# Performance work log

Measured on AMD Instinct MI355X. Metric: run time of the kernel, lower is better.

## Reference

```python
import jax, jax.numpy as jnp
import numpy as np

# ---- constants from init_kwargs ----
RES = 128                       # config.grid.resolution (base_resolution, n_levels=1)
LOG2_T = 22
TABLE_SIZE = 1 << LOG2_T        # hashmap entries
N_G = 4                         # features per level, gaussian grid
N_V = 8                         # features per level, vmf grid
BB_MIN = jnp.array([-10.0, -10.0, -10.0], dtype=jnp.float32)
BB_MAX = jnp.array([10.0, 10.0, 10.0], dtype=jnp.float32)
N_PTS = 1048576

_P2 = np.uint32(2654435761)
_P3 = np.uint32(805459861)
# 8 trilinear corner offsets [8,3]
_CORNERS = jnp.array([[i, j, k] for i in (0, 1) for j in (0, 1) for k in (0, 1)], dtype=jnp.int32)


def hashgrid_lookup(table, pos):
    """tcnn-style HashGrid (1 level, trilinear). pos: [N,3] in [0,1] domain."""
    x = pos * RES                     # scale to grid coords
    x0 = jnp.floor(x)
    w = x - x0                        # [N,3] trilinear weights
    corners = x0.astype(jnp.int32)[:, None, :] + _CORNERS[None]   # [N,8,3]
    cu = corners.astype(jnp.uint32)
    h = (cu[..., 0] ^ (cu[..., 1] * _P2) ^ (cu[..., 2] * _P3)) & jnp.uint32(TABLE_SIZE - 1)
    feat = table[h.astype(jnp.int32)]                              # [N,8,F] gather
    wts = jnp.prod(jnp.where(_CORNERS[None].astype(bool), w[:, None, :], 1.0 - w[:, None, :]), axis=-1)  # [N,8]
    return jnp.einsum('nc,ncf->nf', wts, feat)                     # [N,F]


def sample_vpls(pos, gauss_table, vmf_table):
    """Accumulate encodings over the 27-neighbor stencil (accumulate_gaussians=True)."""
    block = 1.0 / RES
    npos = (pos - BB_MIN) / (BB_MAX - BB_MIN)      # normalized [N,3]
    total_g = jnp.zeros((pos.shape[0], N_G), dtype=jnp.float32)
    total_v = jnp.zeros((pos.shape[0], N_V), dtype=jnp.float32)
    for dx in (-1, 0, 1):
        for dy in (-1, 0, 1):
            for dz in (-1, 0, 1):
                off = jnp.array([dx, dy, dz], dtype=jnp.float32) * block
                p = npos + off
                total_g = total_g + hashgrid_lookup(gauss_table, p)
                total_v = total_v + hashgrid_lookup(vmf_table, p)
    return total_g, total_v


def encode(gaussians, vmf):
    # gaussian_mean_encoding='sigmoid' (non-raw -> rescale to bbox)
    mean = jax.nn.sigmoid(gaussians[:, :3]) * (BB_MAX - BB_MIN) + BB_MIN
    variance = jax.nn.softplus(gaussians[:, 3])[:, None]          # 'softplus'
    sharpness = jnp.exp(vmf[:, 0])[:, None]                        # 'exp'
    ax = vmf[:, 1:4]                                               # 'normalize' (F.normalize, eps=1e-12)
    axis = ax / jnp.maximum(jnp.linalg.norm(ax, axis=1, keepdims=True), 1e-12)
    amplitude = jax.nn.sigmoid(vmf[:, 4:7])                        # 'sigmoid'
    g_out = jnp.concatenate([mean, variance], axis=1)             # [N,4]
    v_out = jnp.concatenate([sharpness, axis, amplitude], axis=1) # [N,7]
    return g_out, v_out


def setup_inputs() -> dict:
    key = jax.random.key(0)
    k1, k2, k3 = jax.random.split(key, 3)
    # world-space query positions inside the bounding box
    u = jax.random.uniform(k1, (N_PTS, 3), dtype=jnp.float32)
    pos = u * (BB_MAX - BB_MIN) + BB_MIN
    # hash-grid feature tables (tcnn initializes near zero)
    gauss_table = jax.random.normal(k2, (TABLE_SIZE, N_G), dtype=jnp.float32) * 0.1
    vmf_table = jax.random.normal(k3, (TABLE_SIZE, N_V), dtype=jnp.float32) * 0.1
    return {"pos": pos, "gauss_table": gauss_table, "vmf_table": vmf_table}


def reference(pos, gauss_table, vmf_table):
    gaussians, vmf = sample_vpls(pos, gauss_table, vmf_table)
    return encode(gaussians, vmf)
```

## Files before the change

### kernel.cpp

```cpp
#include <hip/hip_runtime.h>
#include <hip/hip_fp16.h>
#include <cstdint>

#define TABLE_MASK 0x3FFFFFu
#define P2 2654435761u
#define P3 805459861u

#define XD 128
#define YD 132
#define ZD 132
#define RECU 12
#define NB3 (128 * 128 * 8)
#define SCAN_BLKS (NB3 / 1024)
#define BUILD_BLKS (131 * 66)

__device__ __forceinline__ float sigmoidf_(float x) { return 1.0f / (1.0f + expf(-x)); }

__device__ __forceinline__ uint32_t f2h2(float a, float b) {
    __half2 h = __floats2half2_rn(a, b);
    return *reinterpret_cast<uint32_t*>(&h);
}
__device__ __forceinline__ __half2 u2h2(uint32_t u) {
    return *reinterpret_cast<__half2*>(&u);
}

__device__ __forceinline__ int bin_key3(float px, float py, float pz)
{
    float x = ((px + 10.0f) / 20.0f) * 128.0f;
    float y = ((py + 10.0f) / 20.0f) * 128.0f;
    float z = ((pz + 10.0f) / 20.0f) * 128.0f;
    int ix = min(max((int)floorf(x), 0), 127);
    int iy = min(max((int)floorf(y), 0), 127);
    int iz = min(max((int)floorf(z), 0), 127);
    return (((iz << 7) + iy) << 3) + (ix >> 4);
}

__global__ __launch_bounds__(256)
void build_hist_kernel(const float4* __restrict__ gauss,
                       const float4* __restrict__ vmf,
                       uint32_t* __restrict__ exdx,
                       const float* __restrict__ pos,
                       uint32_t* __restrict__ hist, int n)
{
    if (blockIdx.x >= BUILD_BLKS) {
        int p = (blockIdx.x - BUILD_BLKS) * blockDim.x + threadIdx.x;
        if (p < n) {
            int k = bin_key3(pos[3 * p], pos[3 * p + 1], pos[3 * p + 2]);
            atomicAdd(&hist[k], 1u);
        }
        return;
    }

    __shared__ float sm[2][131][13];
    int bidx = blockIdx.x;
    int yp = bidx % 66;
    int rz = 1 + bidx / 66;
    int ry0 = 1 + 2 * yp;
    int t = threadIdx.x;

    for (int l = t; l < 262; l += 256) {
        int row = (l >= 131) ? 1 : 0;
        int cell = l - row * 131;
        int ry = ry0 + row;
        if (ry <= 131) {
            int xc = 1 + cell;
            uint32_t ux = (uint32_t)(xc - 2);
            uint32_t uy = (uint32_t)(ry - 2);
            uint32_t uz = (uint32_t)(rz - 2);
            uint32_t h = (ux ^ (uy * P2) ^ (uz * P3)) & TABLE_MASK;
            float4 g  = gauss[h];
            float4 v0 = vmf[(size_t)2 * h];
            float4 v1 = vmf[(size_t)2 * h + 1];
            float* s = sm[row][cell];
            s[0] = g.x;  s[1] = g.y;  s[2]  = g.z;  s[3]  = g.w;
            s[4] = v0.x; s[5] = v0.y; s[6]  = v0.z; s[7]  = v0.w;
            s[8] = v1.x; s[9] = v1.y; s[10] = v1.z; s[11] = v1.w;
        }
    }
    __syncthreads();

    int row = t >> 7;
    int c   = t & 127;
    int ry  = ry0 + row;
    if (ry > 131) return;

    uint32_t rec[12];
#pragma unroll
    for (int m = 0; m < 6; ++m) {
        float e0 = sm[row][c][2*m]   + sm[row][c+1][2*m]   + sm[row][c+2][2*m];
        float e1 = sm[row][c][2*m+1] + sm[row][c+1][2*m+1] + sm[row][c+2][2*m+1];
        float d0 = sm[row][c+3][2*m]   - sm[row][c][2*m];
        float d1 = sm[row][c+3][2*m+1] - sm[row][c][2*m+1];
        rec[m]     = f2h2(e0, e1);
        rec[6 + m] = f2h2(d0, d1);
    }
    size_t o = (((size_t)rz * YD + (size_t)ry) * XD + (size_t)c) * RECU;
    *(uint4*)(exdx + o)     = make_uint4(rec[0], rec[1], rec[2],  rec[3]);
    *(uint4*)(exdx + o + 4) = make_uint4(rec[4], rec[5], rec[6],  rec[7]);
    *(uint4*)(exdx + o + 8) = make_uint4(rec[8], rec[9], rec[10], rec[11]);
}

__global__ __launch_bounds__(1024)
void scanA_kernel(const uint32_t* __restrict__ hist,
                  uint32_t* __restrict__ cursor,
                  uint32_t* __restrict__ sums)
{
    __shared__ uint32_t buf[1024];
    int t = threadIdx.x;
    int base = blockIdx.x * 1024;
    uint32_t v = hist[base + t];
    buf[t] = v;
    __syncthreads();
    for (int off = 1; off < 1024; off <<= 1) {
        uint32_t x = (t >= off) ? buf[t - off] : 0u;
        __syncthreads();
        buf[t] += x;
        __syncthreads();
    }
    cursor[base + t] = buf[t] - v;
    if (t == 1023) sums[blockIdx.x] = buf[t];
}

__global__ __launch_bounds__(256)
void scatter_kernel(const float* __restrict__ pos,
                    uint32_t* __restrict__ cursor,
                    const uint32_t* __restrict__ sums,
                    float4* __restrict__ sortedPts, int n)
{
    __shared__ uint32_t soff[SCAN_BLKS];
    int t = threadIdx.x;
    if (t < SCAN_BLKS) soff[t] = sums[t];
    __syncthreads();
    for (int off = 1; off < SCAN_BLKS; off <<= 1) {
        uint32_t v = 0;
        if (t < SCAN_BLKS && t >= off) v = soff[t - off];
        __syncthreads();
        if (t < SCAN_BLKS) soff[t] += v;
        __syncthreads();
    }

    int p = blockIdx.x * blockDim.x + t;
    if (p >= n) return;
    float px = pos[3 * p], py = pos[3 * p + 1], pz = pos[3 * p + 2];
    int k = bin_key3(px, py, pz);
    int chunk = k >> 10;
    uint32_t base = (chunk > 0) ? soff[chunk - 1] : 0u;
    uint32_t slot = base + atomicAdd(&cursor[k], 1u);
    sortedPts[slot] = make_float4(px, py, pz, __uint_as_float((uint32_t)p));
}

__device__ __forceinline__ void consume_cell(const uint4& A, const uint4& B, const uint4& C,
                                             __half2 wxh, float w, float* acc)
{
    uint32_t e[6] = {A.x, A.y, A.z, A.w, B.x, B.y};
    uint32_t d[6] = {B.z, B.w, C.x, C.y, C.z, C.w};
#pragma unroll
    for (int m = 0; m < 6; ++m) {
        __half2 v = __hfma2(wxh, u2h2(d[m]), u2h2(e[m]));
        float2 f = __half22float2(v);
        acc[2*m]     = fmaf(w, f.x, acc[2*m]);
        acc[2*m + 1] = fmaf(w, f.y, acc[2*m + 1]);
    }
}

__global__ __launch_bounds__(256, 2)
void vapl_grid_sorted_kernel(const float4* __restrict__ sortedPts,
                             const uint32_t* __restrict__ exdx,
                             float* __restrict__ out,
                             int n)
{
    int bid = blockIdx.x;
    int nb  = gridDim.x;
    int b2  = ((nb & 7) == 0) ? ((bid & 7) * (nb >> 3) + (bid >> 3)) : bid;
    int s = b2 * (int)blockDim.x + (int)threadIdx.x;
    if (s >= n) return;

    float4 pt = sortedPts[s];
    int p = (int)__float_as_uint(pt.w);

    float x = ((pt.x + 10.0f) / 20.0f) * 128.0f;
    float y = ((pt.y + 10.0f) / 20.0f) * 128.0f;
    float z = ((pt.z + 10.0f) / 20.0f) * 128.0f;

    float fx = floorf(x), fy = floorf(y), fz = floorf(z);
    int ix = (int)fx, iy = (int)fy, iz = (int)fz;
    float wx = x - fx, wy = y - fy, wz = z - fz;

    float ay[4] = {1.0f - wy, 1.0f, 1.0f, wy};
    float az[4] = {1.0f - wz, 1.0f, 1.0f, wz};
    __half2 wxh = __float2half2_rn(wx);

    int bx = ix + 1, by = iy + 1, bz = iz + 1;

    uint32_t idx16[16];
    float    w16[16];
#pragma unroll
    for (int k = 0; k < 4; ++k) {
#pragma unroll
        for (int j = 0; j < 4; ++j) {
            idx16[k*4 + j] = (((uint32_t)(bz + k) * YD + (uint32_t)(by + j)) * XD
                              + (uint32_t)(bx - 1)) * RECU;
            w16[k*4 + j] = ay[j] * az[k];
        }
    }

    float acc[12] = {0.f,0.f,0.f,0.f,0.f,0.f,0.f,0.f,0.f,0.f,0.f,0.f};

    uint4 A[8][3], B[8][3];
#pragma unroll
    for (int c = 0; c < 8; ++c) {
        const uint32_t* r = exdx + idx16[c];
        A[c][0] = *(const uint4*)(r);
        A[c][1] = *(const uint4*)(r + 4);
        A[c][2] = *(const uint4*)(r + 8);
    }
#pragma unroll
    for (int c = 0; c < 8; ++c) {
        const uint32_t* r = exdx + idx16[8 + c];
        B[c][0] = *(const uint4*)(r);
        B[c][1] = *(const uint4*)(r + 4);
        B[c][2] = *(const uint4*)(r + 8);
    }
#pragma unroll
    for (int c = 0; c < 8; ++c)
        consume_cell(A[c][0], A[c][1], A[c][2], wxh, w16[c], acc);
#pragma unroll
    for (int c = 0; c < 8; ++c)
        consume_cell(B[c][0], B[c][1], B[c][2], wxh, w16[8 + c], acc);

    float m0 = sigmoidf_(acc[0]) * 20.0f - 10.0f;
    float m1 = sigmoidf_(acc[1]) * 20.0f - 10.0f;
    float m2 = sigmoidf_(acc[2]) * 20.0f - 10.0f;
    float var = fmaxf(acc[3], 0.0f) + log1pf(expf(-fabsf(acc[3])));

    float sharp = expf(acc[4]);
    float nrm = fmaxf(sqrtf(acc[5]*acc[5] + acc[6]*acc[6] + acc[7]*acc[7]), 1e-12f);
    float a0 = acc[5] / nrm, a1 = acc[6] / nrm, a2 = acc[7] / nrm;
    float amp0 = sigmoidf_(acc[8]);
    float amp1 = sigmoidf_(acc[9]);
    float amp2 = sigmoidf_(acc[10]);

    float* og = out + (size_t)p * 4;
    *(float4*)og = make_float4(m0, m1, m2, var);

    float* ov = out + (size_t)n * 4 + (size_t)p * 7;
    ov[0] = sharp;
    ov[1] = a0;
    ov[2] = a1;
    ov[3] = a2;
    ov[4] = amp0;
    ov[5] = amp1;
    ov[6] = amp2;
}

__global__ __launch_bounds__(256)
void vapl_grid_kernel(const float* __restrict__ pos,
                      const float4* __restrict__ gauss,
                      const float4* __restrict__ vmf,
                      float* __restrict__ out,
                      int n)
{
    int p = blockIdx.x * blockDim.x + threadIdx.x;
    if (p >= n) return;

    float px = pos[3 * p + 0];
    float py = pos[3 * p + 1];
    float pz = pos[3 * p + 2];

    float x = ((px + 10.0f) / 20.0f) * 128.0f;
    float y = ((py + 10.0f) / 20.0f) * 128.0f;
    float z = ((pz + 10.0f) / 20.0f) * 128.0f;

    float fx = floorf(x), fy = floorf(y), fz = floorf(z);
    int ix = (int)fx, iy = (int)fy, iz = (int)fz;
    float wx = x - fx, wy = y - fy, wz = z - fz;

    float ax[4] = {1.0f - wx, 1.0f, 1.0f, wx};
    float ay[4] = {1.0f - wy, 1.0f, 1.0f, wy};
    float az[4] = {1.0f - wz, 1.0f, 1.0f, wz};

    uint32_t hx[4], hy[4], hz[4];
#pragma unroll
    for (int i = 0; i < 4; ++i) {
        hx[i] = (uint32_t)(ix - 1 + i);
        hy[i] = (uint32_t)(iy - 1 + i) * P2;
        hz[i] = (uint32_t)(iz - 1 + i) * P3;
    }

    float tg0 = 0.f, tg1 = 0.f, tg2 = 0.f, tg3 = 0.f;
    float tv0 = 0.f, tv1 = 0.f, tv2 = 0.f, tv3 = 0.f;
    float tv4 = 0.f, tv5 = 0.f, tv6 = 0.f, tv7 = 0.f;

    for (int k = 0; k < 4; ++k) {
        for (int j = 0; j < 4; ++j) {
            uint32_t hyz = hy[j] ^ hz[k];
            float wyz = ay[j] * az[k];
#pragma unroll
            for (int i = 0; i < 4; ++i) {
                uint32_t h = (hx[i] ^ hyz) & TABLE_MASK;
                float w = ax[i] * wyz;
                float4 g  = gauss[h];
                float4 v0 = vmf[(size_t)2 * h];
                float4 v1 = vmf[(size_t)2 * h + 1];
                tg0 = fmaf(w, g.x,  tg0);
                tg1 = fmaf(w, g.y,  tg1);
                tg2 = fmaf(w, g.z,  tg2);
                tg3 = fmaf(w, g.w,  tg3);
                tv0 = fmaf(w, v0.x, tv0);
                tv1 = fmaf(w, v0.y, tv1);
                tv2 = fmaf(w, v0.z, tv2);
                tv3 = fmaf(w, v0.w, tv3);
                tv4 = fmaf(w, v1.x, tv4);
                tv5 = fmaf(w, v1.y, tv5);
                tv6 = fmaf(w, v1.z, tv6);
                tv7 = fmaf(w, v1.w, tv7);
            }
        }
    }

    float m0 = sigmoidf_(tg0) * 20.0f - 10.0f;
    float m1 = sigmoidf_(tg1) * 20.0f - 10.0f;
    float m2 = sigmoidf_(tg2) * 20.0f - 10.0f;
    float var = fmaxf(tg3, 0.0f) + log1pf(expf(-fabsf(tg3)));

    float sharp = expf(tv0);
    float nrm = fmaxf(sqrtf(tv1 * tv1 + tv2 * tv2 + tv3 * tv3), 1e-12f);
    float a0 = tv1 / nrm, a1 = tv2 / nrm, a2 = tv3 / nrm;
    float amp0 = sigmoidf_(tv4);
    float amp1 = sigmoidf_(tv5);
    float amp2 = sigmoidf_(tv6);

    float* og = out + (size_t)p * 4;
    og[0] = m0;
    og[1] = m1;
    og[2] = m2;
    og[3] = var;

    float* ov = out + (size_t)n * 4 + (size_t)p * 7;
    ov[0] = sharp;
    ov[1] = a0;
    ov[2] = a1;
    ov[3] = a2;
    ov[4] = amp0;
    ov[5] = amp1;
    ov[6] = amp2;
}

extern "C" void kernel_launch(void* const* d_in, const int* in_sizes, int n_in,
                              void* d_out, int out_size, void* d_ws, size_t ws_size,
                              hipStream_t stream) {
    const float*  pos   = (const float*)d_in[0];
    const float4* gauss = (const float4*)d_in[1];
    const float4* vmf   = (const float4*)d_in[2];
    float* out = (float*)d_out;
    int n = in_sizes[0] / 3;

    size_t off = 0;
    char* ws = (char*)d_ws;
    uint32_t* exdx   = (uint32_t*)(ws + off);  off += (size_t)XD * YD * ZD * RECU * 4;
    off = (off + 255) & ~(size_t)255;
    uint32_t* hist   = (uint32_t*)(ws + off);  off += (size_t)NB3 * 4;
    uint32_t* cursor = (uint32_t*)(ws + off);  off += (size_t)NB3 * 4;
    uint32_t* sums   = (uint32_t*)(ws + off);  off += 256 * 4;
    off = (off + 255) & ~(size_t)255;
    float4* sortedPts = (float4*)(ws + off);   off += (size_t)n * 16;
    const size_t need = off;

    dim3 block(256);
    dim3 grid((n + 255) / 256);

    if (ws_size >= need) {
        hipMemsetAsync(hist, 0, (size_t)NB3 * 4, stream);
        hipLaunchKernelGGL(build_hist_kernel, dim3(BUILD_BLKS + 4096), block, 0, stream,
                           gauss, vmf, exdx, pos, hist, n);
        hipLaunchKernelGGL(scanA_kernel, dim3(SCAN_BLKS), dim3(1024), 0, stream, hist, cursor, sums);
        hipLaunchKernelGGL(scatter_kernel, grid, block, 0, stream, pos, cursor, sums, sortedPts, n);
        hipLaunchKernelGGL(vapl_grid_sorted_kernel, grid, block, 0, stream,
                           sortedPts, exdx, out, n);
    } else {
        hipLaunchKernelGGL(vapl_grid_kernel, grid, block, 0, stream, pos, gauss, vmf, out, n);
    }
}
```

Before: 260.5 us.

## Bin points into 8^3 tiles and stage tile grid records in LDS

Points are now binned into 4096 coarse 8x8x8 tiles instead of fine x-row bins, and a single-block scan produces per-tile start offsets. The main kernel launches one block per tile, which cooperatively loads the tile's 8x11x11 halo of precomputed half-precision records into shared memory. Each point's 16 stencil records are then read from LDS instead of global memory. This is meant to cut redundant global or L2 traffic for the gathers, at the cost of load imbalance across tiles, a serial single-block scan, and about 46KB of LDS per block that limits occupancy.

Result: slower. 319.2 us (+22.6%).

```diff
diff --git a/kernel.cpp b/kernel.cpp
--- a/kernel.cpp
+++ b/kernel.cpp
@@ -10,8 +10,8 @@
 #define YD 132
 #define ZD 132
 #define RECU 12
-#define NB3 (128 * 128 * 8)
-#define SCAN_BLKS (NB3 / 1024)
+#define NBT 4096
+#define NREC 968
 #define BUILD_BLKS (131 * 66)
 
 __device__ __forceinline__ float sigmoidf_(float x) { return 1.0f / (1.0f + expf(-x)); }
@@ -24,7 +24,7 @@
     return *reinterpret_cast<__half2*>(&u);
 }
 
-__device__ __forceinline__ int bin_key3(float px, float py, float pz)
+__device__ __forceinline__ int bin_tile(float px, float py, float pz)
 {
     float x = ((px + 10.0f) / 20.0f) * 128.0f;
     float y = ((py + 10.0f) / 20.0f) * 128.0f;
@@ -32,7 +32,7 @@
     int ix = min(max((int)floorf(x), 0), 127);
     int iy = min(max((int)floorf(y), 0), 127);
     int iz = min(max((int)floorf(z), 0), 127);
-    return (((iz << 7) + iy) << 3) + (ix >> 4);
+    return ((iz >> 3) << 8) | ((iy >> 3) << 4) | (ix >> 3);
 }
 
 __global__ __launch_bounds__(256)
@@ -45,7 +45,7 @@
     if (blockIdx.x >= BUILD_BLKS) {
         int p = (blockIdx.x - BUILD_BLKS) * blockDim.x + threadIdx.x;
         if (p < n) {
-            int k = bin_key3(pos[3 * p], pos[3 * p + 1], pos[3 * p + 2]);
+            int k = bin_tile(pos[3 * p], pos[3 * p + 1], pos[3 * p + 2]);
             atomicAdd(&hist[k], 1u);
         }
         return;
@@ -101,156 +101,145 @@
 }
 
 __global__ __launch_bounds__(1024)
-void scanA_kernel(const uint32_t* __restrict__ hist,
-                  uint32_t* __restrict__ cursor,
-                  uint32_t* __restrict__ sums)
+void scan4k_kernel(const uint32_t* __restrict__ hist,
+                   uint32_t* __restrict__ cursor,
+                   uint32_t* __restrict__ binStart)
 {
     __shared__ uint32_t buf[1024];
+    __shared__ uint32_t running;
     int t = threadIdx.x;
-    int base = blockIdx.x * 1024;
-    uint32_t v = hist[base + t];
-    buf[t] = v;
+    if (t == 0) running = 0u;
     __syncthreads();
-    for (int off = 1; off < 1024; off <<= 1) {
-        uint32_t x = (t >= off) ? buf[t - off] : 0u;
+    for (int base = 0; base < NBT; base += 1024) {
+        uint32_t v = hist[base + t];
+        buf[t] = v;
         __syncthreads();
-        buf[t] += x;
+        for (int off = 1; off < 1024; off <<= 1) {
+            uint32_t x = (t >= off) ? buf[t - off] : 0u;
+            __syncthreads();
+            buf[t] += x;
+            __syncthreads();
+        }
+        uint32_t incl = buf[t];
+        uint32_t r0 = running;
+        cursor[base + t]   = r0 + incl - v;
+        binStart[base + t] = r0 + incl - v;
         __syncthreads();
-    }
-    cursor[base + t] = buf[t] - v;
-    if (t == 1023) sums[blockIdx.x] = buf[t];
+        if (t == 1023) running = r0 + incl;
+        __syncthreads();
+    }
+    if (t == 0) binStart[NBT] = running;
 }
 
 __global__ __launch_bounds__(256)
 void scatter_kernel(const float* __restrict__ pos,
                     uint32_t* __restrict__ cursor,
-                    const uint32_t* __restrict__ sums,
                     float4* __restrict__ sortedPts, int n)
 {
-    __shared__ uint32_t soff[SCAN_BLKS];
-    int t = threadIdx.x;
-    if (t < SCAN_BLKS) soff[t] = sums[t];
-    __syncthreads();
-    for (int off = 1; off < SCAN_BLKS; off <<= 1) {
-        uint32_t v = 0;
-        if (t < SCAN_BLKS && t >= off) v = soff[t - off];
-        __syncthreads();
-        if (t < SCAN_BLKS) soff[t] += v;
-        __syncthreads();
-    }
-
-    int p = blockIdx.x * blockDim.x + t;
+    int p = blockIdx.x * blockDim.x + threadIdx.x;
     if (p >= n) return;
     float px = pos[3 * p], py = pos[3 * p + 1], pz = pos[3 * p + 2];
-    int k = bin_key3(px, py, pz);
-    int chunk = k >> 10;
-    uint32_t base = (chunk > 0) ? soff[chunk - 1] : 0u;
-    uint32_t slot = base + atomicAdd(&cursor[k], 1u);
+    int k = bin_tile(px, py, pz);
+    uint32_t slot = atomicAdd(&cursor[k], 1u);
     sortedPts[slot] = make_float4(px, py, pz, __uint_as_float((uint32_t)p));
 }
 
-__device__ __forceinline__ void consume_cell(const uint4& A, const uint4& B, const uint4& C,
-                                             __half2 wxh, float w, float* acc)
-{
-    uint32_t e[6] = {A.x, A.y, A.z, A.w, B.x, B.y};
-    uint32_t d[6] = {B.z, B.w, C.x, C.y, C.z, C.w};
-#pragma unroll
-    for (int m = 0; m < 6; ++m) {
-        __half2 v = __hfma2(wxh, u2h2(d[m]), u2h2(e[m]));
-        float2 f = __half22float2(v);
-        acc[2*m]     = fmaf(w, f.x, acc[2*m]);
-        acc[2*m + 1] = fmaf(w, f.y, acc[2*m + 1]);
-    }
-}
-
-__global__ __launch_bounds__(256, 2)
-void vapl_grid_sorted_kernel(const float4* __restrict__ sortedPts,
-                             const uint32_t* __restrict__ exdx,
-                             float* __restrict__ out,
-                             int n)
-{
+__global__ __launch_bounds__(256)
+void vapl_tile_kernel(const float4* __restrict__ sortedPts,
+                      const uint32_t* __restrict__ exdx,
+                      const uint32_t* __restrict__ binStart,
+                      float* __restrict__ out,
+                      int n)
+{
+    __shared__ uint32_t lds[12][NREC];
+
     int bid = blockIdx.x;
-    int nb  = gridDim.x;
-    int b2  = ((nb & 7) == 0) ? ((bid & 7) * (nb >> 3) + (bid >> 3)) : bid;
-    int s = b2 * (int)blockDim.x + (int)threadIdx.x;
-    if (s >= n) return;
-
-    float4 pt = sortedPts[s];
-    int p = (int)__float_as_uint(pt.w);
-
-    float x = ((pt.x + 10.0f) / 20.0f) * 128.0f;
-    float y = ((pt.y + 10.0f) / 20.0f) * 128.0f;
-    float z = ((pt.z + 10.0f) / 20.0f) * 128.0f;
-
-    float fx = floorf(x), fy = floorf(y), fz = floorf(z);
-    int ix = (int)fx, iy = (int)fy, iz = (int)fz;
-    float wx = x - fx, wy = y - fy, wz = z - fz;
-
-    float ay[4] = {1.0f - wy, 1.0f, 1.0f, wy};
-    float az[4] = {1.0f - wz, 1.0f, 1.0f, wz};
-    __half2 wxh = __float2half2_rn(wx);
-
-    int bx = ix + 1, by = iy + 1, bz = iz + 1;
-
-    uint32_t idx16[16];
-    float    w16[16];
-#pragma unroll
-    for (int k = 0; k < 4; ++k) {
-#pragma unroll
-        for (int j = 0; j < 4; ++j) {
-            idx16[k*4 + j] = (((uint32_t)(bz + k) * YD + (uint32_t)(by + j)) * XD
-                              + (uint32_t)(bx - 1)) * RECU;
-            w16[k*4 + j] = ay[j] * az[k];
-        }
-    }
-
-    float acc[12] = {0.f,0.f,0.f,0.f,0.f,0.f,0.f,0.f,0.f,0.f,0.f,0.f};
-
-    uint4 A[8][3], B[8][3];
-#pragma unroll
-    for (int c = 0; c < 8; ++c) {
-        const uint32_t* r = exdx + idx16[c];
-        A[c][0] = *(const uint4*)(r);
-        A[c][1] = *(const uint4*)(r + 4);
-        A[c][2] = *(const uint4*)(r + 8);
-    }
-#pragma unroll
-    for (int c = 0; c < 8; ++c) {
-        const uint32_t* r = exdx + idx16[8 + c];
-        B[c][0] = *(const uint4*)(r);
-        B[c][1] = *(const uint4*)(r + 4);
-        B[c][2] = *(const uint4*)(r + 8);
-    }
-#pragma unroll
-    for (int c = 0; c < 8; ++c)
-        consume_cell(A[c][0], A[c][1], A[c][2], wxh, w16[c], acc);
-#pragma unroll
-    for (int c = 0; c < 8; ++c)
-        consume_cell(B[c][0], B[c][1], B[c][2], wxh, w16[8 + c], acc);
-
-    float m0 = sigmoidf_(acc[0]) * 20.0f - 10.0f;
-    float m1 = sigmoidf_(acc[1]) * 20.0f - 10.0f;
-    float m2 = sigmoidf_(acc[2]) * 20.0f - 10.0f;
-    float var = fmaxf(acc[3], 0.0f) + log1pf(expf(-fabsf(acc[3])));
-
-    float sharp = expf(acc[4]);
-    float nrm = fmaxf(sqrtf(acc[5]*acc[5] + acc[6]*acc[6] + acc[7]*acc[7]), 1e-12f);
-    float a0 = acc[5] / nrm, a1 = acc[6] / nrm, a2 = acc[7] / nrm;
-    float amp0 = sigmoidf_(acc[8]);
-    float amp1 = sigmoidf_(acc[9]);
-    float amp2 = sigmoidf_(acc[10]);
-
-    float* og = out + (size_t)p * 4;
-    *(float4*)og = make_float4(m0, m1, m2, var);
-
-    float* ov = out + (size_t)n * 4 + (size_t)p * 7;
-    ov[0] = sharp;
-    ov[1] = a0;
-    ov[2] = a1;
-    ov[3] = a2;
-    ov[4] = amp0;
-    ov[5] = amp1;
-    ov[6] = amp2;
+    int tile = ((bid & 7) << 9) | (bid >> 3);
+    int tx = tile & 15, ty = (tile >> 4) & 15, tz = tile >> 8;
+
+    int x0  = tx * 8;
+    int cy0 = ty * 8 + 1;
+    int cz0 = tz * 8 + 1;
+    for (int u4 = (int)threadIdx.x; u4 < NREC * 3; u4 += 256) {
+        int rec = u4 / 3;
+        int p   = u4 - rec * 3;
+        int lx  = rec & 7;
+        int t2  = rec >> 3;
+        int ly  = t2 % 11;
+        int lz  = t2 / 11;
+        size_t goff = ((size_t)(cz0 + lz) * YD + (size_t)(cy0 + ly)) * XD + (size_t)(x0 + lx);
+        uint4 v = *(const uint4*)(exdx + goff * RECU + (size_t)p * 4);
+        int q = p * 4;
+        lds[q + 0][rec] = v.x;
+        lds[q + 1][rec] = v.y;
+        lds[q + 2][rec] = v.z;
+        lds[q + 3][rec] = v.w;
+    }
+    __syncthreads();
+
+    int start = (int)binStart[tile];
+    int end   = (int)binStart[tile + 1];
+
+    for (int s = start + (int)threadIdx.x; s < end; s += 256) {
+        float4 pt = sortedPts[s];
+        int p = (int)__float_as_uint(pt.w);
+
+        float x = ((pt.x + 10.0f) / 20.0f) * 128.0f;
+        float y = ((pt.y + 10.0f) / 20.0f) * 128.0f;
+        float z = ((pt.z + 10.0f) / 20.0f) * 128.0f;
+
+        float fx = floorf(x), fy = floorf(y), fz = floorf(z);
+        int ix = (int)fx, iy = (int)fy, iz = (int)fz;
+        float wx = x - fx, wy = y - fy, wz = z - fz;
+
+        float ay[4] = {1.0f - wy, 1.0f, 1.0f, wy};
+        float az[4] = {1.0f - wz, 1.0f, 1.0f, wz};
+        __half2 wxh = __float2half2_rn(wx);
+
+        int r0 = (ix - x0) + 8 * ((iy - ty * 8) + 11 * (iz - tz * 8));
+
+        float acc[12] = {0.f,0.f,0.f,0.f,0.f,0.f,0.f,0.f,0.f,0.f,0.f,0.f};
+#pragma unroll
+        for (int k = 0; k < 4; ++k) {
+            float azk = az[k];
+#pragma unroll
+            for (int j = 0; j < 4; ++j) {
+                int r = r0 + 8 * j + 88 * k;
+                float w = ay[j] * azk;
+#pragma unroll
+                for (int m = 0; m < 6; ++m) {
+                    __half2 v = __hfma2(wxh, u2h2(lds[6 + m][r]), u2h2(lds[m][r]));
+                    float2 f = __half22float2(v);
+                    acc[2*m]     = fmaf(w, f.x, acc[2*m]);
+                    acc[2*m + 1] = fmaf(w, f.y, acc[2*m + 1]);
+                }
+            }
+        }
+
+        float m0 = sigmoidf_(acc[0]) * 20.0f - 10.0f;
+        float m1 = sigmoidf_(acc[1]) * 20.0f - 10.0f;
+        float m2 = sigmoidf_(acc[2]) * 20.0f - 10.0f;
+        float var = fmaxf(acc[3], 0.0f) + log1pf(expf(-fabsf(acc[3])));
+
+        float sharp = expf(acc[4]);
+        float nrm = fmaxf(sqrtf(acc[5]*acc[5] + acc[6]*acc[6] + acc[7]*acc[7]), 1e-12f);
+        float a0 = acc[5] / nrm, a1 = acc[6] / nrm, a2 = acc[7] / nrm;
+        float amp0 = sigmoidf_(acc[8]);
+        float amp1 = sigmoidf_(acc[9]);
+        float amp2 = sigmoidf_(acc[10]);
+
+        float* og = out + (size_t)p * 4;
+        *(float4*)og = make_float4(m0, m1, m2, var);
+
+        float* ov = out + (size_t)n * 4 + (size_t)p * 7;
+        ov[0] = sharp;
+        ov[1] = a0;
+        ov[2] = a1;
+        ov[3] = a2;
+        ov[4] = amp0;
+        ov[5] = amp1;
+        ov[6] = amp2;
+    }
 }
 
 __global__ __launch_bounds__(256)
@@ -357,26 +346,26 @@
 
     size_t off = 0;
     char* ws = (char*)d_ws;
-    uint32_t* exdx   = (uint32_t*)(ws + off);  off += (size_t)XD * YD * ZD * RECU * 4;
+    uint32_t* exdx     = (uint32_t*)(ws + off);  off += (size_t)XD * YD * ZD * RECU * 4;
     off = (off + 255) & ~(size_t)255;
-    uint32_t* hist   = (uint32_t*)(ws + off);  off += (size_t)NB3 * 4;
-    uint32_t* cursor = (uint32_t*)(ws + off);  off += (size_t)NB3 * 4;
-    uint32_t* sums   = (uint32_t*)(ws + off);  off += 256 * 4;
+    uint32_t* hist     = (uint32_t*)(ws + off);  off += (size_t)NBT * 4;
+    uint32_t* cursor   = (uint32_t*)(ws + off);  off += (size_t)NBT * 4;
+    uint32_t* binStart = (uint32_t*)(ws + off);  off += (size_t)(NBT + 1) * 4;
     off = (off + 255) & ~(size_t)255;
-    float4* sortedPts = (float4*)(ws + off);   off += (size_t)n * 16;
+    float4* sortedPts  = (float4*)(ws + off);    off += (size_t)n * 16;
     const size_t need = off;
 
     dim3 block(256);
     dim3 grid((n + 255) / 256);
 
     if (ws_size >= need) {
-        hipMemsetAsync(hist, 0, (size_t)NB3 * 4, stream);
+        hipMemsetAsync(hist, 0, (size_t)NBT * 4, stream);
         hipLaunchKernelGGL(build_hist_kernel, dim3(BUILD_BLKS + 4096), block, 0, stream,
                            gauss, vmf, exdx, pos, hist, n);
-        hipLaunchKernelGGL(scanA_kernel, dim3(SCAN_BLKS), dim3(1024), 0, stream, hist, cursor, sums);
-        hipLaunchKernelGGL(scatter_kernel, grid, block, 0, stream, pos, cursor, sums, sortedPts, n);
-        hipLaunchKernelGGL(vapl_grid_sorted_kernel, grid, block, 0, stream,
-                           sortedPts, exdx, out, n);
+        hipLaunchKernelGGL(scan4k_kernel, dim3(1), dim3(1024), 0, stream, hist, cursor, binStart);
+        hipLaunchKernelGGL(scatter_kernel, grid, block, 0, stream, pos, cursor, sortedPts, n);
+        hipLaunchKernelGGL(vapl_tile_kernel, dim3(NBT), block, 0, stream,
+                           sortedPts, exdx, binStart, out, n);
     } else {
         hipLaunchKernelGGL(vapl_grid_kernel, grid, block, 0, stream, pos, gauss, vmf, out, n);
     }
```

## Split each point across four threads with interleaved padded precomputed records

Applied to the files above, without the earlier changes.

The precomputed per-cell record is padded from 12 to 16 words and interleaved so each quarter holds paired (sum, difference) half2 values for four features. The final kernel now assigns four threads per point: each thread loads one 16-byte slice from the 16 stencil cells and accumulates four features, and three of the four lanes finish the output activations. This cuts per-thread register pressure and gives contiguous 64-byte per-point reads, in exchange for four times as many threads, redundant per-point coordinate math, one idle lane in four, and a larger table to build and write.

Measured after the change: 309.4 us. 1.19x slower.

```diff
diff --git a/kernel.cpp b/kernel.cpp
--- a/kernel.cpp
+++ b/kernel.cpp
@@ -9,7 +9,7 @@
 #define XD 128
 #define YD 132
 #define ZD 132
-#define RECU 12
+#define RECU 16
 #define NB3 (128 * 128 * 8)
 #define SCAN_BLKS (NB3 / 1024)
 #define BUILD_BLKS (131 * 66)
@@ -84,20 +84,21 @@
     int ry  = ry0 + row;
     if (ry > 131) return;
 
-    uint32_t rec[12];
+    uint32_t ex[6], dx[6];
 #pragma unroll
     for (int m = 0; m < 6; ++m) {
         float e0 = sm[row][c][2*m]   + sm[row][c+1][2*m]   + sm[row][c+2][2*m];
         float e1 = sm[row][c][2*m+1] + sm[row][c+1][2*m+1] + sm[row][c+2][2*m+1];
         float d0 = sm[row][c+3][2*m]   - sm[row][c][2*m];
         float d1 = sm[row][c+3][2*m+1] - sm[row][c][2*m+1];
-        rec[m]     = f2h2(e0, e1);
-        rec[6 + m] = f2h2(d0, d1);
+        ex[m] = f2h2(e0, e1);
+        dx[m] = f2h2(d0, d1);
     }
     size_t o = (((size_t)rz * YD + (size_t)ry) * XD + (size_t)c) * RECU;
-    *(uint4*)(exdx + o)     = make_uint4(rec[0], rec[1], rec[2],  rec[3]);
-    *(uint4*)(exdx + o + 4) = make_uint4(rec[4], rec[5], rec[6],  rec[7]);
-    *(uint4*)(exdx + o + 8) = make_uint4(rec[8], rec[9], rec[10], rec[11]);
+    *(uint4*)(exdx + o)      = make_uint4(ex[0], dx[0], ex[1], dx[1]);
+    *(uint4*)(exdx + o + 4)  = make_uint4(ex[2], dx[2], ex[3], dx[3]);
+    *(uint4*)(exdx + o + 8)  = make_uint4(ex[4], dx[4], ex[5], dx[5]);
+    *(uint4*)(exdx + o + 12) = make_uint4(0u, 0u, 0u, 0u);
 }
 
 __global__ __launch_bounds__(1024)
@@ -149,33 +150,20 @@
     sortedPts[slot] = make_float4(px, py, pz, __uint_as_float((uint32_t)p));
 }
 
-__device__ __forceinline__ void consume_cell(const uint4& A, const uint4& B, const uint4& C,
-                                             __half2 wxh, float w, float* acc)
-{
-    uint32_t e[6] = {A.x, A.y, A.z, A.w, B.x, B.y};
-    uint32_t d[6] = {B.z, B.w, C.x, C.y, C.z, C.w};
-#pragma unroll
-    for (int m = 0; m < 6; ++m) {
-        __half2 v = __hfma2(wxh, u2h2(d[m]), u2h2(e[m]));
-        float2 f = __half22float2(v);
-        acc[2*m]     = fmaf(w, f.x, acc[2*m]);
-        acc[2*m + 1] = fmaf(w, f.y, acc[2*m + 1]);
-    }
-}
-
 __global__ __launch_bounds__(256, 2)
-void vapl_grid_sorted_kernel(const float4* __restrict__ sortedPts,
-                             const uint32_t* __restrict__ exdx,
-                             float* __restrict__ out,
-                             int n)
+void vapl_group_kernel(const float4* __restrict__ sortedPts,
+                       const uint32_t* __restrict__ exdx,
+                       float* __restrict__ out,
+                       int n)
 {
     int bid = blockIdx.x;
     int nb  = gridDim.x;
     int b2  = ((nb & 7) == 0) ? ((bid & 7) * (nb >> 3) + (bid >> 3)) : bid;
-    int s = b2 * (int)blockDim.x + (int)threadIdx.x;
-    if (s >= n) return;
-
-    float4 pt = sortedPts[s];
+    int g   = b2 * 64 + ((int)threadIdx.x >> 2);
+    if (g >= n) return;
+    int r = (int)threadIdx.x & 3;
+
+    float4 pt = sortedPts[g];
     int p = (int)__float_as_uint(pt.w);
 
     float x = ((pt.x + 10.0f) / 20.0f) * 128.0f;
@@ -192,65 +180,55 @@
 
     int bx = ix + 1, by = iy + 1, bz = iz + 1;
 
-    uint32_t idx16[16];
-    float    w16[16];
+    uint4 u[16];
 #pragma unroll
     for (int k = 0; k < 4; ++k) {
 #pragma unroll
         for (int j = 0; j < 4; ++j) {
-            idx16[k*4 + j] = (((uint32_t)(bz + k) * YD + (uint32_t)(by + j)) * XD
-                              + (uint32_t)(bx - 1)) * RECU;
-            w16[k*4 + j] = ay[j] * az[k];
-        }
-    }
-
-    float acc[12] = {0.f,0.f,0.f,0.f,0.f,0.f,0.f,0.f,0.f,0.f,0.f,0.f};
-
-    uint4 A[8][3], B[8][3];
-#pragma unroll
-    for (int c = 0; c < 8; ++c) {
-        const uint32_t* r = exdx + idx16[c];
-        A[c][0] = *(const uint4*)(r);
-        A[c][1] = *(const uint4*)(r + 4);
-        A[c][2] = *(const uint4*)(r + 8);
-    }
-#pragma unroll
-    for (int c = 0; c < 8; ++c) {
-        const uint32_t* r = exdx + idx16[8 + c];
-        B[c][0] = *(const uint4*)(r);
-        B[c][1] = *(const uint4*)(r + 4);
-        B[c][2] = *(const uint4*)(r + 8);
-    }
-#pragma unroll
-    for (int c = 0; c < 8; ++c)
-        consume_cell(A[c][0], A[c][1], A[c][2], wxh, w16[c], acc);
-#pragma unroll
-    for (int c = 0; c < 8; ++c)
-        consume_cell(B[c][0], B[c][1], B[c][2], wxh, w16[8 + c], acc);
-
-    float m0 = sigmoidf_(acc[0]) * 20.0f - 10.0f;
-    float m1 = sigmoidf_(acc[1]) * 20.0f - 10.0f;
-    float m2 = sigmoidf_(acc[2]) * 20.0f - 10.0f;
-    float var = fmaxf(acc[3], 0.0f) + log1pf(expf(-fabsf(acc[3])));
-
-    float sharp = expf(acc[4]);
-    float nrm = fmaxf(sqrtf(acc[5]*acc[5] + acc[6]*acc[6] + acc[7]*acc[7]), 1e-12f);
-    float a0 = acc[5] / nrm, a1 = acc[6] / nrm, a2 = acc[7] / nrm;
-    float amp0 = sigmoidf_(acc[8]);
-    float amp1 = sigmoidf_(acc[9]);
-    float amp2 = sigmoidf_(acc[10]);
-
-    float* og = out + (size_t)p * 4;
-    *(float4*)og = make_float4(m0, m1, m2, var);
-
-    float* ov = out + (size_t)n * 4 + (size_t)p * 7;
-    ov[0] = sharp;
-    ov[1] = a0;
-    ov[2] = a1;
-    ov[3] = a2;
-    ov[4] = amp0;
-    ov[5] = amp1;
-    ov[6] = amp2;
+            size_t cell = ((size_t)(bz + k) * YD + (size_t)(by + j)) * XD + (size_t)(bx - 1);
+            u[k * 4 + j] = *(const uint4*)(exdx + cell * RECU + (size_t)(r * 4));
+        }
+    }
+
+    float a0 = 0.f, a1 = 0.f, a2 = 0.f, a3 = 0.f;
+#pragma unroll
+    for (int k = 0; k < 4; ++k) {
+        float azk = az[k];
+#pragma unroll
+        for (int j = 0; j < 4; ++j) {
+            float w = ay[j] * azk;
+            uint4 v = u[k * 4 + j];
+            __half2 t0 = __hfma2(wxh, u2h2(v.y), u2h2(v.x));
+            __half2 t1 = __hfma2(wxh, u2h2(v.w), u2h2(v.z));
+            float2 f0 = __half22float2(t0);
+            float2 f1 = __half22float2(t1);
+            a0 = fmaf(w, f0.x, a0);
+            a1 = fmaf(w, f0.y, a1);
+            a2 = fmaf(w, f1.x, a2);
+            a3 = fmaf(w, f1.y, a3);
+        }
+    }
+
+    if (r == 0) {
+        float m0 = sigmoidf_(a0) * 20.0f - 10.0f;
+        float m1 = sigmoidf_(a1) * 20.0f - 10.0f;
+        float m2 = sigmoidf_(a2) * 20.0f - 10.0f;
+        float var = fmaxf(a3, 0.0f) + log1pf(expf(-fabsf(a3)));
+        *(float4*)(out + (size_t)p * 4) = make_float4(m0, m1, m2, var);
+    } else if (r == 1) {
+        float sharp = expf(a0);
+        float nrm = fmaxf(sqrtf(a1 * a1 + a2 * a2 + a3 * a3), 1e-12f);
+        float* ov = out + (size_t)n * 4 + (size_t)p * 7;
+        ov[0] = sharp;
+        ov[1] = a1 / nrm;
+        ov[2] = a2 / nrm;
+        ov[3] = a3 / nrm;
+    } else if (r == 2) {
+        float* ov = out + (size_t)n * 4 + (size_t)p * 7;
+        ov[4] = sigmoidf_(a0);
+        ov[5] = sigmoidf_(a1);
+        ov[6] = sigmoidf_(a2);
+    }
 }
 
 __global__ __launch_bounds__(256)
@@ -375,7 +353,8 @@
                            gauss, vmf, exdx, pos, hist, n);
         hipLaunchKernelGGL(scanA_kernel, dim3(SCAN_BLKS), dim3(1024), 0, stream, hist, cursor, sums);
         hipLaunchKernelGGL(scatter_kernel, grid, block, 0, stream, pos, cursor, sums, sortedPts, n);
-        hipLaunchKernelGGL(vapl_grid_sorted_kernel, grid, block, 0, stream,
+        dim3 ggrid((unsigned)((n + 63) / 64));
+        hipLaunchKernelGGL(vapl_group_kernel, ggrid, block, 0, stream,
                            sortedPts, exdx, out, n);
     } else {
         hipLaunchKernelGGL(vapl_grid_kernel, grid, block, 0, stream, pos, gauss, vmf, out, n);
```
